# Kernel optimization log

Hardware: AMD Instinct MI355X
Metric: run time of the kernel (lower is better)

Reference implementation:

```python
import jax, jax.numpy as jnp
import numpy as np
from jax import lax

VOCAB, EMB, H, L_CTX = 5, 64, 256, 100
HG = 2 * H  # generator hidden = 512


def lstm_cell(x, h, c, Wih, Whh, b):
    # PyTorch gate order: i, f, g, o
    z = x @ Wih.T + h @ Whh.T + b
    i, f, g, o = jnp.split(z, 4, axis=-1)
    c = jax.nn.sigmoid(f) * c + jax.nn.sigmoid(i) * jnp.tanh(g)
    h = jax.nn.sigmoid(o) * jnp.tanh(c)
    return h, c


def run_lstm(xs, Wih, Whh, b, hidden):
    # xs: [T, B, D] -> ys: [T, B, hidden]
    B = xs.shape[1]
    h0 = jnp.zeros((B, hidden), xs.dtype)

    def step(carry, x):
        h, c = carry
        h, c = lstm_cell(x, h, c, Wih, Whh, b)
        return (h, c), h

    _, ys = lax.scan(step, (h0, h0), xs)
    return ys


def bidir_layer(xs, Wih, Whh, b):
    # Wih/Whh/b stacked over directions: [2, ...]
    yf = run_lstm(xs, Wih[0], Whh[0], b[0], H)
    yb = run_lstm(xs[::-1], Wih[1], Whh[1], b[1], H)[::-1]
    return jnp.concatenate([yf, yb], axis=-1)  # [T, B, 2H]


def setup_inputs() -> dict:
    key = jax.random.key(0)
    ks = iter(jax.random.split(key, 24))
    s = 1.0 / np.sqrt(H)  # pytorch-style uniform scale -> use normal*s

    def w(shape):
        return (jax.random.normal(next(ks), shape, jnp.float32) * s).astype(jnp.float32)

    B = 1024
    inp = {
        "left_context": jax.random.randint(next(ks), (B, L_CTX), 0, VOCAB),
        "right_context": jax.random.randint(next(ks), (B, L_CTX), 0, VOCAB),
        "target_length": 256,
        "emb": w((VOCAB, EMB)),
        # bidirectional context LSTM, layer 0 (in=64) and layer 1 (in=512)
        "ctx0_Wih": w((2, 4 * H, EMB)),
        "ctx0_Whh": w((2, 4 * H, H)),
        "ctx0_b": w((2, 4 * H)),
        "ctx1_Wih": w((2, 4 * H, 2 * H)),
        "ctx1_Whh": w((2, 4 * H, H)),
        "ctx1_b": w((2, 4 * H)),
        # generator LSTM (hidden=512), layer 0 (in=64) and layer 1 (in=512)
        "gen0_Wih": w((4 * HG, EMB)),
        "gen0_Whh": w((4 * HG, HG)),
        "gen0_b": w((4 * HG,)),
        "gen1_Wih": w((4 * HG, HG)),
        "gen1_Whh": w((4 * HG, HG)),
        "gen1_b": w((4 * HG,)),
        "out_W": w((VOCAB, HG)),
        "out_b": w((VOCAB,)),
    }
    return inp


def reference(left_context, right_context, target_length, emb,
              ctx0_Wih, ctx0_Whh, ctx0_b, ctx1_Wih, ctx1_Whh, ctx1_b,
              gen0_Wih, gen0_Whh, gen0_b, gen1_Wih, gen1_Whh, gen1_b,
              out_W, out_b):
    B = left_context.shape[0]

    def encode(tokens):
        x = emb[tokens].transpose(1, 0, 2)          # [L, B, 64]
        x = bidir_layer(x, ctx0_Wih, ctx0_Whh, ctx0_b)  # dropout: eval -> identity
        x = bidir_layer(x, ctx1_Wih, ctx1_Whh, ctx1_b)
        return x                                     # [L, B, 512]

    left_final = encode(left_context)[-1]            # [B, 512]
    right_final = encode(right_context)[0]           # [B, 512]
    combined = (left_final + right_final) * 0.5

    # h_0 = combined repeated over both generator layers; c_0 = 0
    zeros = jnp.zeros((B, HG), combined.dtype)
    tok0 = jnp.zeros((B,), jnp.int32)

    def dec_step(carry, _):
        h0, c0, h1, c1, tok = carry
        x = emb[tok]                                 # [B, 64]
        h0, c0 = lstm_cell(x, h0, c0, gen0_Wih, gen0_Whh, gen0_b)
        h1, c1 = lstm_cell(h0, h1, c1, gen1_Wih, gen1_Whh, gen1_b)
        logits = h1 @ out_W.T + out_b                # dropout: eval -> identity
        tok = jnp.argmax(logits, axis=-1)
        return (h0, c0, h1, c1, tok), logits

    _, logits = lax.scan(dec_step, (combined, zeros, combined, zeros, tok0),
                         None, length=target_length)
    return logits.transpose(1, 0, 2)                 # [B, T, vocab]
```

## Files before the change

### kernel.cpp

```cpp
#include <hip/hip_runtime.h>


#define L_SEQ 100
#define BATCH 1024
#define HCTX 256
#define HG 512
#define TDEC 256

typedef __attribute__((ext_vector_type(8))) short bf16x8;
typedef __attribute__((ext_vector_type(4))) float f32x4;

__device__ __forceinline__ float sigf(float x){ return 1.0f/(1.0f+expf(-x)); }
__device__ __forceinline__ unsigned short f2bf(float x){
  unsigned int u = __float_as_uint(x);
  return (unsigned short)((u + 0x7fffu + ((u>>16)&1u)) >> 16);
}
__device__ __forceinline__ float bf2f(unsigned short h){
  return __uint_as_float(((unsigned int)h)<<16);
}

__global__ void pack_w(const float* __restrict__ W, int G, int K, int KTtot, int kt0,
                       unsigned short* __restrict__ hi, unsigned short* __restrict__ lo){
  int idx = blockIdx.x*blockDim.x + threadIdx.x;
  int kt_n = K/32;
  int total = (G/16)*kt_n*64;
  if (idx >= total) return;
  int lane = idx & 63;
  int ktl = (idx>>6) % kt_n;
  int gt  = (idx>>6) / kt_n;
  int g = gt*16 + (lane & 15);
  int k = ktl*32 + (lane>>4)*8;
  const float* src = W + (size_t)g*K + k;
  size_t dst = (((size_t)gt*KTtot + (kt0 + ktl))*64 + lane)*8;
  #pragma unroll
  for (int j=0;j<8;j++){
    float x = src[j];
    unsigned short h = f2bf(x);
    hi[dst+j] = h;
    lo[dst+j] = f2bf(x - bf2f(h));
  }
}

__global__ void embprep(const float* __restrict__ emb,
                        const float* __restrict__ c0Wih, const float* __restrict__ c0b,
                        const float* __restrict__ g0Wih, const float* __restrict__ g0b,
                        float* __restrict__ ectx0, float* __restrict__ egen0){
  int idx = blockIdx.x*blockDim.x + threadIdx.x;
  if (idx < 2*5*1024){
    int d = idx / 5120;
    int v = (idx / 1024) % 5;
    int j = idx % 1024;
    const float* w = c0Wih + ((size_t)d*1024 + j)*64;
    const float* e = emb + v*64;
    float s = c0b[d*1024 + j];
    #pragma unroll
    for (int k=0;k<64;k++) s += e[k]*w[k];
    ectx0[idx] = s;
  } else if (idx < 2*5*1024 + 5*2048){
    int i2 = idx - 10240;
    int v = i2 / 2048;
    int j = i2 % 2048;
    const float* w = g0Wih + (size_t)j*64;
    const float* e = emb + v*64;
    float s = g0b[j];
    #pragma unroll
    for (int k=0;k<64;k++) s += e[k]*w[k];
    egen0[i2] = s;
  }
}

__global__ void __launch_bounds__(512,1) ctx_l0_mfma(
    const int* __restrict__ toks,
    const float* __restrict__ ectx0,
    const unsigned short* __restrict__ wh, const unsigned short* __restrict__ wl,
    unsigned short* __restrict__ y0h, unsigned short* __restrict__ y0l)
{
  const int id  = blockIdx.x;
  const int dir = (id >> 2) & 1;
  const int bx  = ((id >> 3) << 2) | (id & 3);
  const int e0  = bx * 16;
  const int lane = threadIdx.x & 63;
  const int w    = threadIdx.x >> 6;
  const int lo16 = lane & 15, kgrp = lane >> 4;

  __shared__ unsigned short hsh[16*256];
  __shared__ unsigned short hsl[16*256];
  __shared__ float cs[16*256];
  for (int i=threadIdx.x;i<16*256;i+=512){ hsh[i]=0; hsl[i]=0; cs[i]=0.f; }
  __syncthreads();

  const unsigned short* pbh[4][2];
  const unsigned short* pbl[4][2];
  #pragma unroll
  for (int g=0;g<4;g++){
    #pragma unroll
    for (int st=0;st<2;st++){
      int ct = g*16 + w*2 + st;
      size_t off = (size_t)dir*1024*256 + ((size_t)(ct*8)*64 + lane)*8;
      pbh[g][st] = wh + off; pbl[g][st] = wl + off;
    }
  }
  const unsigned aoff0 = (unsigned)(lo16*512 + kgrp*16);
  const unsigned axor  = ((unsigned)(lo16 & 7)) << 4;

  for (int s=0;s<L_SEQ;s++){
    const int t = dir ? (L_SEQ-1-s) : s;
    f32x4 zero = {0.f,0.f,0.f,0.f};
    f32x4 acc[4][2];
    #pragma unroll
    for (int g=0;g<4;g++){
      #pragma unroll
      for (int st=0;st<2;st++) acc[g][st] = zero;
    }
    #pragma unroll 2
    for (int kt=0;kt<8;kt++){
      unsigned ao = (aoff0 + kt*64) ^ axor;
      bf16x8 ah = *(const bf16x8*)((const char*)hsh + ao);
      bf16x8 al = *(const bf16x8*)((const char*)hsl + ao);
      #pragma unroll
      for (int g=0;g<4;g++){
        #pragma unroll
        for (int st=0;st<2;st++){
          bf16x8 bh = *(const bf16x8*)(pbh[g][st] + (size_t)kt*512);
          bf16x8 bl = *(const bf16x8*)(pbl[g][st] + (size_t)kt*512);
          acc[g][st] = __builtin_amdgcn_mfma_f32_16x16x32_bf16(ah,bh,acc[g][st],0,0,0);
          acc[g][st] = __builtin_amdgcn_mfma_f32_16x16x32_bf16(al,bh,acc[g][st],0,0,0);
          acc[g][st] = __builtin_amdgcn_mfma_f32_16x16x32_bf16(ah,bl,acc[g][st],0,0,0);
        }
      }
    }
    __syncthreads();
    int tkr[4];
    #pragma unroll
    for (int r=0;r<4;r++) tkr[r] = toks[(e0 + kgrp*4 + r)*L_SEQ + t];
    #pragma unroll
    for (int st=0;st<2;st++){
      const int unit = w*32 + st*16 + lo16;
      #pragma unroll
      for (int r=0;r<4;r++){
        const int row = kgrp*4 + r;
        const int e = e0 + row;
        const float* ep = ectx0 + ((size_t)(dir*5 + tkr[r]))*1024 + unit;
        float zi = acc[0][st][r] + ep[0];
        float zf = acc[1][st][r] + ep[256];
        float zg = acc[2][st][r] + ep[512];
        float zo = acc[3][st][r] + ep[768];
        int ci = row*256 + unit;
        float c = sigf(zf)*cs[ci] + sigf(zi)*tanhf(zg);
        float h = sigf(zo)*tanhf(c);
        cs[ci] = c;
        unsigned short hb = f2bf(h), lb = f2bf(h - bf2f(hb));
        unsigned hoff = ((unsigned)(row*512 + unit*2)) ^ (((unsigned)(row & 7)) << 4);
        *(unsigned short*)((char*)hsh + hoff) = hb;
        *(unsigned short*)((char*)hsl + hoff) = lb;
        size_t yo = ((size_t)t*BATCH + e)*512 + dir*256 + unit;
        y0h[yo] = hb; y0l[yo] = lb;
      }
    }
    __syncthreads();
  }
}

__global__ void __launch_bounds__(512,1) ctx_l1_mfma(
    const unsigned short* __restrict__ y0h, const unsigned short* __restrict__ y0l,
    const unsigned short* __restrict__ wh, const unsigned short* __restrict__ wl,
    const float* __restrict__ bias,
    float* __restrict__ finals, int t_store)
{
  const int id  = blockIdx.x;
  const int dir = (id >> 2) & 1;
  const int bx  = ((id >> 3) << 2) | (id & 3);
  const int e0  = bx * 16;
  const int lane = threadIdx.x & 63;
  const int w    = threadIdx.x >> 6;
  const int lo16 = lane & 15, kgrp = lane >> 4;

  __shared__ unsigned short xsh[16*512];
  __shared__ unsigned short xsl[16*512];
  __shared__ unsigned short hsh[16*256];
  __shared__ unsigned short hsl[16*256];
  __shared__ float cs[16*256];
  for (int i=threadIdx.x;i<16*256;i+=512){ hsh[i]=0; hsl[i]=0; cs[i]=0.f; }

  float bb[4][2];
  #pragma unroll
  for (int g=0;g<4;g++){
    #pragma unroll
    for (int st=0;st<2;st++)
      bb[g][st] = bias[dir*1024 + g*256 + w*32 + st*16 + lo16];
  }
  const unsigned short* pbh[4][2];
  const unsigned short* pbl[4][2];
  #pragma unroll
  for (int g=0;g<4;g++){
    #pragma unroll
    for (int st=0;st<2;st++){
      int ct = g*16 + w*2 + st;
      size_t off = (size_t)dir*1024*768 + ((size_t)(ct*24)*64 + lane)*8;
      pbh[g][st] = wh + off; pbl[g][st] = wl + off;
    }
  }
  const unsigned axor = ((unsigned)(lo16 & 7)) << 4;
  __syncthreads();

  for (int s=0;s<L_SEQ;s++){
    const int t = dir ? (L_SEQ-1-s) : s;
    #pragma unroll
    for (int cc=0; cc<2; cc++){
      int ci = threadIdx.x + cc*512;
      int row = ci >> 6, cr = ci & 63;
      const unsigned short* srcbase = y0h + ((size_t)t*BATCH + e0 + row)*512 + cr*8;
      const unsigned short* srcbasel = y0l + ((size_t)t*BATCH + e0 + row)*512 + cr*8;
      uint4 vh = *(const uint4*)srcbase;
      uint4 vl = *(const uint4*)srcbasel;
      unsigned xo = ((unsigned)(row*1024 + cr*16)) ^ (((unsigned)(row & 7)) << 4);
      *(uint4*)((char*)xsh + xo) = vh;
      *(uint4*)((char*)xsl + xo) = vl;
    }
    __syncthreads();
    f32x4 zero = {0.f,0.f,0.f,0.f};
    f32x4 acc[4][2];
    #pragma unroll
    for (int g=0;g<4;g++){
      #pragma unroll
      for (int st=0;st<2;st++) acc[g][st] = zero;
    }
    #pragma unroll 2
    for (int kt=0;kt<16;kt++){
      unsigned ao = ((unsigned)(lo16*1024 + kt*64 + kgrp*16)) ^ axor;
      bf16x8 ah = *(const bf16x8*)((const char*)xsh + ao);
      bf16x8 al = *(const bf16x8*)((const char*)xsl + ao);
      #pragma unroll
      for (int g=0;g<4;g++){
        #pragma unroll
        for (int st=0;st<2;st++){
          bf16x8 bh = *(const bf16x8*)(pbh[g][st] + (size_t)kt*512);
          bf16x8 bl = *(const bf16x8*)(pbl[g][st] + (size_t)kt*512);
          acc[g][st] = __builtin_amdgcn_mfma_f32_16x16x32_bf16(ah,bh,acc[g][st],0,0,0);
          acc[g][st] = __builtin_amdgcn_mfma_f32_16x16x32_bf16(al,bh,acc[g][st],0,0,0);
          acc[g][st] = __builtin_amdgcn_mfma_f32_16x16x32_bf16(ah,bl,acc[g][st],0,0,0);
        }
      }
    }
    #pragma unroll 2
    for (int kt=16;kt<24;kt++){
      unsigned ao = ((unsigned)(lo16*512 + (kt-16)*64 + kgrp*16)) ^ axor;
      bf16x8 ah = *(const bf16x8*)((const char*)hsh + ao);
      bf16x8 al = *(const bf16x8*)((const char*)hsl + ao);
      #pragma unroll
      for (int g=0;g<4;g++){
        #pragma unroll
        for (int st=0;st<2;st++){
          bf16x8 bh = *(const bf16x8*)(pbh[g][st] + (size_t)kt*512);
          bf16x8 bl = *(const bf16x8*)(pbl[g][st] + (size_t)kt*512);
          acc[g][st] = __builtin_amdgcn_mfma_f32_16x16x32_bf16(ah,bh,acc[g][st],0,0,0);
          acc[g][st] = __builtin_amdgcn_mfma_f32_16x16x32_bf16(al,bh,acc[g][st],0,0,0);
          acc[g][st] = __builtin_amdgcn_mfma_f32_16x16x32_bf16(ah,bl,acc[g][st],0,0,0);
        }
      }
    }
    __syncthreads();
    #pragma unroll
    for (int st=0;st<2;st++){
      const int unit = w*32 + st*16 + lo16;
      #pragma unroll
      for (int r=0;r<4;r++){
        const int row = kgrp*4 + r;
        float zi = acc[0][st][r] + bb[0][st];
        float zf = acc[1][st][r] + bb[1][st];
        float zg = acc[2][st][r] + bb[2][st];
        float zo = acc[3][st][r] + bb[3][st];
        int ci = row*256 + unit;
        float c = sigf(zf)*cs[ci] + sigf(zi)*tanhf(zg);
        float h = sigf(zo)*tanhf(c);
        cs[ci] = c;
        unsigned short hb = f2bf(h), lb = f2bf(h - bf2f(hb));
        unsigned hoff = ((unsigned)(row*512 + unit*2)) ^ (((unsigned)(row & 7)) << 4);
        *(unsigned short*)((char*)hsh + hoff) = hb;
        *(unsigned short*)((char*)hsl + hoff) = lb;
        if (t == t_store)
          finals[(size_t)(e0 + row)*512 + dir*256 + unit] = h;
      }
    }
    __syncthreads();
  }
}

__global__ void combine_init2(const float* __restrict__ lf, const float* __restrict__ rf,
                              unsigned short* __restrict__ h0h, unsigned short* __restrict__ h0l,
                              unsigned short* __restrict__ h1h, unsigned short* __restrict__ h1l,
                              float* __restrict__ c0, float* __restrict__ c1){
  int i = blockIdx.x*blockDim.x + threadIdx.x;
  if (i < BATCH*HG){
    float v = 0.5f*(lf[i]+rf[i]);
    unsigned short h = f2bf(v);
    unsigned short l = f2bf(v - bf2f(h));
    h0h[i]=h; h0l[i]=l; h1h[i]=h; h1l[i]=l;
    c0[i]=0.f; c1[i]=0.f;
  }
}

__global__ void __launch_bounds__(512,1) dec_l0_mfma(
    const float* __restrict__ egen0,
    const unsigned short* __restrict__ wh, const unsigned short* __restrict__ wl,
    const unsigned short* __restrict__ hih, const unsigned short* __restrict__ hil,
    const unsigned short* __restrict__ h1ih, const unsigned short* __restrict__ h1il,
    unsigned short* __restrict__ hoh, unsigned short* __restrict__ hol,
    float* __restrict__ cst,
    const float* __restrict__ outW, const float* __restrict__ outb,
    float* __restrict__ out, int t)
{
  const int bid = blockIdx.x;
  const int by = bid & 15;
  const int bx = bid >> 4;
  const int e0 = bx * 64;
  const int lane = threadIdx.x & 63;
  const int w = threadIdx.x >> 6;
  const int wm = w & 3, wu = w >> 2;
  const int ut = by*2 + wu;
  const int lo16 = lane & 15, kgrp = lane >> 4;
  const int arow = e0 + wm*16 + lo16;
  const int u = ut*16 + lo16;
  const int r0 = e0 + wm*16 + kgrp*4;

  const unsigned short* pah = hih + (size_t)arow*512 + kgrp*8;
  const unsigned short* pal = hil + (size_t)arow*512 + kgrp*8;
  const unsigned short* pb[8];
  #pragma unroll
  for (int q=0;q<4;q++){
    size_t off = ((size_t)(q*32+ut)*16*64 + lane)*8;
    pb[q]   = wh + off;
    pb[q+4] = wl + off;
  }
  const f32x4 z4 = {0.f,0.f,0.f,0.f};
  f32x4 aHH[4]={z4,z4,z4,z4}, aLH[4]={z4,z4,z4,z4}, aHL[4]={z4,z4,z4,z4};

  #pragma unroll 2
  for (int ks=0; ks<16; ks++){
    bf16x8 ah = *(const bf16x8*)(pah + (size_t)ks*32);
    bf16x8 al = *(const bf16x8*)(pal + (size_t)ks*32);
    #pragma unroll
    for (int q=0;q<4;q++){
      bf16x8 bh = *(const bf16x8*)(pb[q]   + (size_t)ks*512);
      bf16x8 bl = *(const bf16x8*)(pb[q+4] + (size_t)ks*512);
      aHH[q] = __builtin_amdgcn_mfma_f32_16x16x32_bf16(ah, bh, aHH[q], 0,0,0);
      aLH[q] = __builtin_amdgcn_mfma_f32_16x16x32_bf16(al, bh, aLH[q], 0,0,0);
      aHL[q] = __builtin_amdgcn_mfma_f32_16x16x32_bf16(ah, bl, aHL[q], 0,0,0);
    }
  }

  int tkr[4] = {0,0,0,0};
  if (t > 0){
    float acc5[4][5];
    #pragma unroll
    for (int r=0;r<4;r++){
      #pragma unroll
      for (int v=0;v<5;v++) acc5[r][v]=0.f;
    }
    #pragma unroll
    for (int j=0;j<4;j++){
      const int ub = lo16*32 + j*8;
      f32x4 w0[5], w1[5];
      #pragma unroll
      for (int v=0;v<5;v++){
        const float* wp = outW + v*512 + ub;
        w0[v] = *(const f32x4*)(wp);
        w1[v] = *(const f32x4*)(wp+4);
      }
      #pragma unroll
      for (int r=0;r<4;r++){
        const unsigned short* hh = h1ih + (size_t)(r0+r)*512 + ub;
        const unsigned short* hl = h1il + (size_t)(r0+r)*512 + ub;
        bf16x8 vh = *(const bf16x8*)hh;
        bf16x8 vl = *(const bf16x8*)hl;
        #pragma unroll
        for (int m=0;m<4;m++){
          float hv = bf2f((unsigned short)vh[m]) + bf2f((unsigned short)vl[m]);
          #pragma unroll
          for (int v=0;v<5;v++) acc5[r][v] += hv * w0[v][m];
        }
        #pragma unroll
        for (int m=0;m<4;m++){
          float hv = bf2f((unsigned short)vh[m+4]) + bf2f((unsigned short)vl[m+4]);
          #pragma unroll
          for (int v=0;v<5;v++) acc5[r][v] += hv * w1[v][m];
        }
      }
    }
    #pragma unroll
    for (int r=0;r<4;r++){
      #pragma unroll
      for (int v=0;v<5;v++){
        float s = acc5[r][v];
        s += __shfl_xor(s, 1);
        s += __shfl_xor(s, 2);
        s += __shfl_xor(s, 4);
        s += __shfl_xor(s, 8);
        acc5[r][v] = s + outb[v];
      }
      float best = acc5[r][0]; int tk = 0;
      if (acc5[r][1] > best){ best = acc5[r][1]; tk = 1; }
      if (acc5[r][2] > best){ best = acc5[r][2]; tk = 2; }
      if (acc5[r][3] > best){ best = acc5[r][3]; tk = 3; }
      if (acc5[r][4] > best){ best = acc5[r][4]; tk = 4; }
      tkr[r] = tk;
    }
    if (by == 0 && wu == 0 && lo16 == 0){
      #pragma unroll
      for (int r=0;r<4;r++){
        float* op = out + ((size_t)(r0+r)*TDEC + (t-1))*5;
        #pragma unroll
        for (int v=0;v<5;v++) op[v] = acc5[r][v];
      }
    }
  }

  #pragma unroll
  for (int r=0;r<4;r++){
    const int e = r0 + r;
    const float* ep = egen0 + (size_t)tkr[r]*2048 + u;
    float zi = aHH[0][r]+aLH[0][r]+aHL[0][r] + ep[0];
    float zf = aHH[1][r]+aLH[1][r]+aHL[1][r] + ep[512];
    float zg = aHH[2][r]+aLH[2][r]+aHL[2][r] + ep[1024];
    float zo = aHH[3][r]+aLH[3][r]+aHL[3][r] + ep[1536];
    const size_t idx = (size_t)e*512 + u;
    float c = sigf(zf)*cst[idx] + sigf(zi)*tanhf(zg);
    float h = sigf(zo)*tanhf(c);
    cst[idx] = c;
    unsigned short hb = f2bf(h);
    hoh[idx] = hb;
    hol[idx] = f2bf(h - bf2f(hb));
  }
}

__global__ void __launch_bounds__(512,1) dec_l1_mfma(
    const unsigned short* __restrict__ xh, const unsigned short* __restrict__ xl,
    const unsigned short* __restrict__ wh, const unsigned short* __restrict__ wl,
    const float* __restrict__ bias,
    const unsigned short* __restrict__ hih, const unsigned short* __restrict__ hil,
    unsigned short* __restrict__ hoh, unsigned short* __restrict__ hol,
    float* __restrict__ cst)
{
  const int bid = blockIdx.x;
  const int by = bid & 15;
  const int bx = bid >> 4;
  const int e0 = bx * 64;
  const int lane = threadIdx.x & 63;
  const int w = threadIdx.x >> 6;
  const int wm = w & 3, wu = w >> 2;
  const int ut = by*2 + wu;
  const int lo16 = lane & 15, kgrp = lane >> 4;
  const int arow = e0 + wm*16 + lo16;
  const int u = ut*16 + lo16;
  const int r0 = e0 + wm*16 + kgrp*4;

  const unsigned short* pxh = xh  + (size_t)arow*512 + kgrp*8;
  const unsigned short* pxl = xl  + (size_t)arow*512 + kgrp*8;
  const unsigned short* pah = hih + (size_t)arow*512 + kgrp*8;
  const unsigned short* pal = hil + (size_t)arow*512 + kgrp*8;
  const unsigned short* pb[8];
  #pragma unroll
  for (int q=0;q<4;q++){
    size_t off = ((size_t)(q*32+ut)*32*64 + lane)*8;
    pb[q]   = wh + off;
    pb[q+4] = wl + off;
  }
  const f32x4 z4 = {0.f,0.f,0.f,0.f};
  f32x4 aHH[4]={z4,z4,z4,z4}, aLH[4]={z4,z4,z4,z4}, aHL[4]={z4,z4,z4,z4};

  #pragma unroll 2
  for (int ks=0; ks<16; ks++){
    bf16x8 ah = *(const bf16x8*)(pxh + (size_t)ks*32);
    bf16x8 al = *(const bf16x8*)(pxl + (size_t)ks*32);
    #pragma unroll
    for (int q=0;q<4;q++){
      bf16x8 bh = *(const bf16x8*)(pb[q]   + (size_t)ks*512);
      bf16x8 bl = *(const bf16x8*)(pb[q+4] + (size_t)ks*512);
      aHH[q] = __builtin_amdgcn_mfma_f32_16x16x32_bf16(ah, bh, aHH[q], 0,0,0);
      aLH[q] = __builtin_amdgcn_mfma_f32_16x16x32_bf16(al, bh, aLH[q], 0,0,0);
      aHL[q] = __builtin_amdgcn_mfma_f32_16x16x32_bf16(ah, bl, aHL[q], 0,0,0);
    }
  }
  #pragma unroll 2
  for (int ks=16; ks<32; ks++){
    bf16x8 ah = *(const bf16x8*)(pah + (size_t)(ks-16)*32);
    bf16x8 al = *(const bf16x8*)(pal + (size_t)(ks-16)*32);
    #pragma unroll
    for (int q=0;q<4;q++){
      bf16x8 bh = *(const bf16x8*)(pb[q]   + (size_t)ks*512);
      bf16x8 bl = *(const bf16x8*)(pb[q+4] + (size_t)ks*512);
      aHH[q] = __builtin_amdgcn_mfma_f32_16x16x32_bf16(ah, bh, aHH[q], 0,0,0);
      aLH[q] = __builtin_amdgcn_mfma_f32_16x16x32_bf16(al, bh, aLH[q], 0,0,0);
      aHL[q] = __builtin_amdgcn_mfma_f32_16x16x32_bf16(ah, bl, aHL[q], 0,0,0);
    }
  }

  const float b0 = bias[u], b1 = bias[512+u], b2 = bias[1024+u], b3 = bias[1536+u];
  #pragma unroll
  for (int r=0;r<4;r++){
    const int e = r0 + r;
    float zi = aHH[0][r]+aLH[0][r]+aHL[0][r] + b0;
    float zf = aHH[1][r]+aLH[1][r]+aHL[1][r] + b1;
    float zg = aHH[2][r]+aLH[2][r]+aHL[2][r] + b2;
    float zo = aHH[3][r]+aLH[3][r]+aHL[3][r] + b3;
    const size_t idx = (size_t)e*512 + u;
    float c = sigf(zf)*cst[idx] + sigf(zi)*tanhf(zg);
    float h = sigf(zo)*tanhf(c);
    cst[idx] = c;
    unsigned short hb = f2bf(h);
    hoh[idx] = hb;
    hol[idx] = f2bf(h - bf2f(hb));
  }
}

__global__ void dec_outF(const unsigned short* __restrict__ h1h,
                         const unsigned short* __restrict__ h1l,
                         const float* __restrict__ outW,
                         const float* __restrict__ outb,
                         float* __restrict__ out){
  const int lane = threadIdx.x & 63;
  const int e = blockIdx.x*4 + (threadIdx.x >> 6);
  const unsigned short* hh = h1h + (size_t)e*512;
  const unsigned short* hl = h1l + (size_t)e*512;
  float s0=0,s1=0,s2=0,s3=0,s4=0;
  for (int k=lane;k<512;k+=64){
    float hv = bf2f(hh[k]) + bf2f(hl[k]);
    s0 += hv*outW[k];
    s1 += hv*outW[512+k];
    s2 += hv*outW[1024+k];
    s3 += hv*outW[1536+k];
    s4 += hv*outW[2048+k];
  }
  #pragma unroll
  for (int off=32; off>0; off>>=1){
    s0 += __shfl_down(s0, off);
    s1 += __shfl_down(s1, off);
    s2 += __shfl_down(s2, off);
    s3 += __shfl_down(s3, off);
    s4 += __shfl_down(s4, off);
  }
  if (lane==0){
    float* op = out + ((size_t)e*TDEC + (TDEC-1))*5;
    op[0]=s0+outb[0]; op[1]=s1+outb[1]; op[2]=s2+outb[2];
    op[3]=s3+outb[3]; op[4]=s4+outb[4];
  }
}

extern "C" void kernel_launch(void* const* d_in, const int* in_sizes, int n_in,
                              void* d_out, int out_size, void* d_ws, size_t ws_size,
                              hipStream_t stream){
  (void)in_sizes; (void)n_in; (void)out_size;
  const int*   leftc    = (const int*)d_in[0];
  const int*   rightc   = (const int*)d_in[1];
  const float* emb      = (const float*)d_in[3];
  const float* ctx0_Wih = (const float*)d_in[4];
  const float* ctx0_Whh = (const float*)d_in[5];
  const float* ctx0_b   = (const float*)d_in[6];
  const float* ctx1_Wih = (const float*)d_in[7];
  const float* ctx1_Whh = (const float*)d_in[8];
  const float* ctx1_b   = (const float*)d_in[9];
  const float* gen0_Wih = (const float*)d_in[10];
  const float* gen0_Whh = (const float*)d_in[11];
  const float* gen0_b   = (const float*)d_in[12];
  const float* gen1_Wih = (const float*)d_in[13];
  const float* gen1_Whh = (const float*)d_in[14];
  const float* gen1_b   = (const float*)d_in[15];
  const float* out_W    = (const float*)d_in[16];
  const float* out_b    = (const float*)d_in[17];
  float* out = (float*)d_out;

  char* p = (char*)d_ws;
  auto carve = [&](size_t nfloats)->float*{
    float* r = (float*)p;
    p += ((nfloats*sizeof(float) + 255) & ~(size_t)255);
    return r;
  };
  auto carveu = [&](size_t nush)->unsigned short*{
    return (unsigned short*)carve((nush + 1)/2);
  };
  float* ectx0  = carve(2*5*1024);
  float* egen0  = carve(5*2048);
  float* leftF  = carve((size_t)BATCH*HG);
  float* rightF = carve((size_t)BATCH*HG);
  float* c0s    = carve((size_t)BATCH*HG);
  float* c1s    = carve((size_t)BATCH*HG);
  unsigned short* c0pkh = carveu((size_t)2*1024*256);
  unsigned short* c0pkl = carveu((size_t)2*1024*256);
  unsigned short* c1pkh = carveu((size_t)2*1024*768);
  unsigned short* c1pkl = carveu((size_t)2*1024*768);
  unsigned short* pk0h = carveu((size_t)2048*512);
  unsigned short* pk0l = carveu((size_t)2048*512);
  unsigned short* pk1h = carveu((size_t)2048*1024);
  unsigned short* pk1l = carveu((size_t)2048*1024);
  unsigned short* h0ha = carveu((size_t)BATCH*HG);
  unsigned short* h0la = carveu((size_t)BATCH*HG);
  unsigned short* h0hb = carveu((size_t)BATCH*HG);
  unsigned short* h0lb = carveu((size_t)BATCH*HG);
  unsigned short* h1ha = carveu((size_t)BATCH*HG);
  unsigned short* h1la = carveu((size_t)BATCH*HG);
  unsigned short* h1hb = carveu((size_t)BATCH*HG);
  unsigned short* h1lb = carveu((size_t)BATCH*HG);
  unsigned short* y0h = carveu((size_t)L_SEQ*BATCH*512);
  unsigned short* y0l = carveu((size_t)L_SEQ*BATCH*512);
  if ((size_t)(p - (char*)d_ws) > ws_size) return;

  for (int d=0; d<2; d++){
    pack_w<<<128, 256, 0, stream>>>(ctx0_Whh + (size_t)d*1024*256, 1024, 256, 8, 0,
                                    c0pkh + (size_t)d*262144, c0pkl + (size_t)d*262144);
    pack_w<<<256, 256, 0, stream>>>(ctx1_Wih + (size_t)d*1024*512, 1024, 512, 24, 0,
                                    c1pkh + (size_t)d*786432, c1pkl + (size_t)d*786432);
    pack_w<<<128, 256, 0, stream>>>(ctx1_Whh + (size_t)d*1024*256, 1024, 256, 24, 16,
                                    c1pkh + (size_t)d*786432, c1pkl + (size_t)d*786432);
  }
  pack_w<<<512, 256, 0, stream>>>(gen0_Whh, 2048, 512, 16,  0, pk0h, pk0l);
  pack_w<<<512, 256, 0, stream>>>(gen1_Wih, 2048, 512, 32,  0, pk1h, pk1l);
  pack_w<<<512, 256, 0, stream>>>(gen1_Whh, 2048, 512, 32, 16, pk1h, pk1l);

  embprep<<<(20480+255)/256, 256, 0, stream>>>(emb, ctx0_Wih, ctx0_b,
                                               gen0_Wih, gen0_b, ectx0, egen0);

  ctx_l0_mfma<<<128, 512, 0, stream>>>(leftc, ectx0, c0pkh, c0pkl, y0h, y0l);
  ctx_l1_mfma<<<128, 512, 0, stream>>>(y0h, y0l, c1pkh, c1pkl, ctx1_b, leftF, L_SEQ-1);
  ctx_l0_mfma<<<128, 512, 0, stream>>>(rightc, ectx0, c0pkh, c0pkl, y0h, y0l);
  ctx_l1_mfma<<<128, 512, 0, stream>>>(y0h, y0l, c1pkh, c1pkl, ctx1_b, rightF, 0);

  combine_init2<<<(BATCH*HG+255)/256, 256, 0, stream>>>(leftF, rightF,
                                                        h0ha, h0la, h1ha, h1la,
                                                        c0s, c1s);

  for (int t=0;t<TDEC;t++){
    unsigned short* h0ih = (t&1)? h0hb : h0ha;
    unsigned short* h0il = (t&1)? h0lb : h0la;
    unsigned short* h0oh = (t&1)? h0ha : h0hb;
    unsigned short* h0ol = (t&1)? h0la : h0lb;
    unsigned short* h1ih = (t&1)? h1hb : h1ha;
    unsigned short* h1il = (t&1)? h1lb : h1la;
    unsigned short* h1oh = (t&1)? h1ha : h1hb;
    unsigned short* h1ol = (t&1)? h1la : h1lb;
    dec_l0_mfma<<<256, 512, 0, stream>>>(egen0, pk0h, pk0l,
                                         h0ih, h0il, h1ih, h1il,
                                         h0oh, h0ol, c0s,
                                         out_W, out_b, out, t);
    dec_l1_mfma<<<256, 512, 0, stream>>>(h0oh, h0ol, pk1h, pk1l, gen1_b,
                                         h1ih, h1il, h1oh, h1ol, c1s);
  }
  dec_outF<<<256, 256, 0, stream>>>(h1ha, h1la, out_W, out_b, out);
}
```

Before: 28.06 ms.

## Stage decoder weight tiles in LDS with double-buffered async global loads

The decoder LSTM kernels now copy the packed bf16 hi/lo weight fragments into a double-buffered shared-memory tile with global_load_lds, prefetching the next K chunk while MFMAs consume the current one. Before, every wave loaded its weight fragments directly from global memory. The intent is to cut duplicated global weight traffic across the four M-waves sharing the same gate columns and to hide load latency behind compute. In exchange it uses 128KB of LDS per block and adds a __syncthreads per chunk, and there is no explicit vmcnt wait before the barrier, which may be a correctness risk.

Measured after the change: 22.96 ms. 18.2% less time.

```diff
diff --git a/kernel.cpp b/kernel.cpp
--- a/kernel.cpp
+++ b/kernel.cpp
@@ -310,6 +310,7 @@
     const float* __restrict__ outW, const float* __restrict__ outb,
     float* __restrict__ out, int t)
 {
+  __shared__ unsigned short bsm[2][32768];
   const int bid = blockIdx.x;
   const int by = bid & 15;
   const int bx = bid >> 4;
@@ -325,28 +326,47 @@
 
   const unsigned short* pah = hih + (size_t)arow*512 + kgrp*8;
   const unsigned short* pal = hil + (size_t)arow*512 + kgrp*8;
-  const unsigned short* pb[8];
-  #pragma unroll
-  for (int q=0;q<4;q++){
-    size_t off = ((size_t)(q*32+ut)*16*64 + lane)*8;
-    pb[q]   = wh + off;
-    pb[q+4] = wl + off;
-  }
+
+  auto STAGE = [&](int c){
+    #pragma unroll
+    for (int i=0;i<8;i++){
+      int id = w*8 + i;
+      int hl  = id & 1;
+      int q   = (id >> 1) & 3;
+      int wu2 = (id >> 3) & 1;
+      int ksl = id >> 4;
+      int ks  = c*4 + ksl;
+      const unsigned short* src = (hl ? wl : wh)
+          + (((size_t)(q*32 + by*2 + wu2)*16 + ks)*64 + lane)*8;
+      __builtin_amdgcn_global_load_lds((const void*)src,
+          (void*)(&bsm[c & 1][id*512]), 16, 0, 0);
+    }
+  };
+
   const f32x4 z4 = {0.f,0.f,0.f,0.f};
   f32x4 aHH[4]={z4,z4,z4,z4}, aLH[4]={z4,z4,z4,z4}, aHL[4]={z4,z4,z4,z4};
 
-  #pragma unroll 2
-  for (int ks=0; ks<16; ks++){
-    bf16x8 ah = *(const bf16x8*)(pah + (size_t)ks*32);
-    bf16x8 al = *(const bf16x8*)(pal + (size_t)ks*32);
-    #pragma unroll
-    for (int q=0;q<4;q++){
-      bf16x8 bh = *(const bf16x8*)(pb[q]   + (size_t)ks*512);
-      bf16x8 bl = *(const bf16x8*)(pb[q+4] + (size_t)ks*512);
-      aHH[q] = __builtin_amdgcn_mfma_f32_16x16x32_bf16(ah, bh, aHH[q], 0,0,0);
-      aLH[q] = __builtin_amdgcn_mfma_f32_16x16x32_bf16(al, bh, aLH[q], 0,0,0);
-      aHL[q] = __builtin_amdgcn_mfma_f32_16x16x32_bf16(ah, bl, aHL[q], 0,0,0);
-    }
+  STAGE(0);
+  __syncthreads();
+  for (int c=0; c<4; c++){
+    if (c+1 < 4) STAGE(c+1);
+    const unsigned short* bb = &bsm[c&1][0];
+    #pragma unroll
+    for (int ksl=0; ksl<4; ksl++){
+      int ks = c*4 + ksl;
+      bf16x8 ah = *(const bf16x8*)(pah + (size_t)ks*32);
+      bf16x8 al = *(const bf16x8*)(pal + (size_t)ks*32);
+      #pragma unroll
+      for (int q=0;q<4;q++){
+        int fid = ((ksl*2 + wu)*4 + q)*2;
+        bf16x8 bh = *(const bf16x8*)(bb + fid*512     + lane*8);
+        bf16x8 bl = *(const bf16x8*)(bb + fid*512+512 + lane*8);
+        aHH[q] = __builtin_amdgcn_mfma_f32_16x16x32_bf16(ah, bh, aHH[q], 0,0,0);
+        aLH[q] = __builtin_amdgcn_mfma_f32_16x16x32_bf16(al, bh, aLH[q], 0,0,0);
+        aHL[q] = __builtin_amdgcn_mfma_f32_16x16x32_bf16(ah, bl, aHL[q], 0,0,0);
+      }
+    }
+    __syncthreads();
   }
 
   int tkr[4] = {0,0,0,0};
@@ -441,6 +461,7 @@
     unsigned short* __restrict__ hoh, unsigned short* __restrict__ hol,
     float* __restrict__ cst)
 {
+  __shared__ unsigned short bsm[2][32768];
   const int bid = blockIdx.x;
   const int by = bid & 15;
   const int bx = bid >> 4;
@@ -458,41 +479,49 @@
   const unsigned short* pxl = xl  + (size_t)arow*512 + kgrp*8;
   const unsigned short* pah = hih + (size_t)arow*512 + kgrp*8;
   const unsigned short* pal = hil + (size_t)arow*512 + kgrp*8;
-  const unsigned short* pb[8];
-  #pragma unroll
-  for (int q=0;q<4;q++){
-    size_t off = ((size_t)(q*32+ut)*32*64 + lane)*8;
-    pb[q]   = wh + off;
-    pb[q+4] = wl + off;
-  }
+
+  auto STAGE = [&](int c){
+    #pragma unroll
+    for (int i=0;i<8;i++){
+      int id = w*8 + i;
+      int hl  = id & 1;
+      int q   = (id >> 1) & 3;
+      int wu2 = (id >> 3) & 1;
+      int ksl = id >> 4;
+      int ks  = c*4 + ksl;
+      const unsigned short* src = (hl ? wl : wh)
+          + (((size_t)(q*32 + by*2 + wu2)*32 + ks)*64 + lane)*8;
+      __builtin_amdgcn_global_load_lds((const void*)src,
+          (void*)(&bsm[c & 1][id*512]), 16, 0, 0);
+    }
+  };
+
   const f32x4 z4 = {0.f,0.f,0.f,0.f};
   f32x4 aHH[4]={z4,z4,z4,z4}, aLH[4]={z4,z4,z4,z4}, aHL[4]={z4,z4,z4,z4};
 
-  #pragma unroll 2
-  for (int ks=0; ks<16; ks++){
-    bf16x8 ah = *(const bf16x8*)(pxh + (size_t)ks*32);
-    bf16x8 al = *(const bf16x8*)(pxl + (size_t)ks*32);
-    #pragma unroll
-    for (int q=0;q<4;q++){
-      bf16x8 bh = *(const bf16x8*)(pb[q]   + (size_t)ks*512);
-      bf16x8 bl = *(const bf16x8*)(pb[q+4] + (size_t)ks*512);
-      aHH[q] = __builtin_amdgcn_mfma_f32_16x16x32_bf16(ah, bh, aHH[q], 0,0,0);
-      aLH[q] = __builtin_amdgcn_mfma_f32_16x16x32_bf16(al, bh, aLH[q], 0,0,0);
-      aHL[q] = __builtin_amdgcn_mfma_f32_16x16x32_bf16(ah, bl, aHL[q], 0,0,0);
-    }
-  }
-  #pragma unroll 2
-  for (int ks=16; ks<32; ks++){
-    bf16x8 ah = *(const bf16x8*)(pah + (size_t)(ks-16)*32);
-    bf16x8 al = *(const bf16x8*)(pal + (size_t)(ks-16)*32);
-    #pragma unroll
-    for (int q=0;q<4;q++){
-      bf16x8 bh = *(const bf16x8*)(pb[q]   + (size_t)ks*512);
-      bf16x8 bl = *(const bf16x8*)(pb[q+4] + (size_t)ks*512);
-      aHH[q] = __builtin_amdgcn_mfma_f32_16x16x32_bf16(ah, bh, aHH[q], 0,0,0);
-      aLH[q] = __builtin_amdgcn_mfma_f32_16x16x32_bf16(al, bh, aLH[q], 0,0,0);
-      aHL[q] = __builtin_amdgcn_mfma_f32_16x16x32_bf16(ah, bl, aHL[q], 0,0,0);
-    }
+  STAGE(0);
+  __syncthreads();
+  for (int c=0; c<8; c++){
+    if (c+1 < 8) STAGE(c+1);
+    const unsigned short* bb = &bsm[c&1][0];
+    const unsigned short* pAh = (c < 4) ? pxh : pah;
+    const unsigned short* pAl = (c < 4) ? pxl : pal;
+    const int ksA = (c & 3)*4;
+    #pragma unroll
+    for (int ksl=0; ksl<4; ksl++){
+      bf16x8 ah = *(const bf16x8*)(pAh + (size_t)(ksA+ksl)*32);
+      bf16x8 al = *(const bf16x8*)(pAl + (size_t)(ksA+ksl)*32);
+      #pragma unroll
+      for (int q=0;q<4;q++){
+        int fid = ((ksl*2 + wu)*4 + q)*2;
+        bf16x8 bh = *(const bf16x8*)(bb + fid*512     + lane*8);
+        bf16x8 bl = *(const bf16x8*)(bb + fid*512+512 + lane*8);
+        aHH[q] = __builtin_amdgcn_mfma_f32_16x16x32_bf16(ah, bh, aHH[q], 0,0,0);
+        aLH[q] = __builtin_amdgcn_mfma_f32_16x16x32_bf16(al, bh, aLH[q], 0,0,0);
+        aHL[q] = __builtin_amdgcn_mfma_f32_16x16x32_bf16(ah, bl, aHL[q], 0,0,0);
+      }
+    }
+    __syncthreads();
   }
 
   const float b0 = bias[u], b1 = bias[512+u], b2 = bias[1024+u], b3 = bias[1536+u];
```
